# Performance work log

Hardware: AMD Instinct MI355X
Metric: run time of the kernel (lower is better)

The kernel has to match this reference:

```python
import jax, jax.numpy as jnp
import numpy as np

N, C, H, W = 8, 256, 128, 128   # images, AE-error channels, feature map size
A = 3                            # anchors per location (3 aspect ratios)
G = 64                           # GT boxes per image
STRIDE = 8
ANCHOR_SIZE = 32.0
ASPECT_RATIOS = (0.5, 1.0, 2.0)
UNK_CLASS = 80
D = 64                           # density_dim


def make_anchors():
    # detectron2 DefaultAnchorGenerator: cell anchors + grid shifts, (H, W, A) order, A fastest
    r = jnp.asarray(ASPECT_RATIOS, jnp.float32)
    w = ANCHOR_SIZE / jnp.sqrt(r)
    h = ANCHOR_SIZE * jnp.sqrt(r)
    cell = jnp.stack([-w / 2, -h / 2, w / 2, h / 2], axis=1)          # [A,4]
    sx = jnp.arange(W, dtype=jnp.float32) * STRIDE
    sy = jnp.arange(H, dtype=jnp.float32) * STRIDE
    yy, xx = jnp.meshgrid(sy, sx, indexing='ij')
    shifts = jnp.stack([xx, yy, xx, yy], axis=-1).reshape(-1, 4)      # [H*W,4]
    return (shifts[:, None, :] + cell[None, :, :]).reshape(-1, 4)     # [H*W*A,4]


def pairwise_iou(boxes, anchors):
    # boxes [G,4], anchors [R,4] -> [G,R]
    area_b = (boxes[:, 2] - boxes[:, 0]) * (boxes[:, 3] - boxes[:, 1])
    area_a = (anchors[:, 2] - anchors[:, 0]) * (anchors[:, 3] - anchors[:, 1])
    lt = jnp.maximum(boxes[:, None, :2], anchors[None, :, :2])
    rb = jnp.minimum(boxes[:, None, 2:], anchors[None, :, 2:])
    wh = jnp.clip(rb - lt, 0.0)
    inter = wh[..., 0] * wh[..., 1]
    return inter / jnp.maximum(area_b[:, None] + area_a[None, :] - inter, 1e-9)


def setup_inputs() -> dict:
    key = jax.random.key(0)
    k = jax.random.split(key, 9)
    err = jax.random.normal(k[0], (N, C, H, W), jnp.float32)
    err_map = jax.random.normal(k[1], (N, 1, H, W), jnp.float32)
    cxy = jax.random.uniform(k[2], (N, G, 2), minval=0.0, maxval=float(H * STRIDE))
    wh = jax.random.uniform(k[3], (N, G, 2), minval=16.0, maxval=128.0)
    gt_boxes = jnp.concatenate([cxy - wh / 2, cxy + wh / 2], axis=-1)
    gt_classes = jax.random.randint(k[4], (N, G), 0, 81, dtype=jnp.int32)
    w1 = jax.random.normal(k[5], (1, D), jnp.float32) * 0.5
    b1 = jnp.zeros((D,), jnp.float32)
    w2 = jax.random.normal(k[6], (D, D // 2), jnp.float32) * (1.0 / np.sqrt(D))
    b2 = jnp.zeros((D // 2,), jnp.float32)
    w3 = jax.random.normal(k[7], (D // 2, 1), jnp.float32) * (1.0 / np.sqrt(D // 2))
    b3 = jnp.zeros((1,), jnp.float32)
    return dict(err=err, err_map=err_map, gt_boxes=gt_boxes, w1=w1, b1=b1,
                w2=w2, b2=b2, w3=w3, b3=b3, gt_classes=gt_classes)


def reference(err, err_map, gt_boxes, w1, b1, w2, b2, w3, b3, gt_classes):
    # loss_ae: mean of squared flattened per-anchor errors (mean is permutation invariant)
    loss_ae = jnp.mean(err ** 2)

    # density head on every error-map pixel: Linear(1,D)-ReLU-Linear(D,D/2)-ReLU-Linear(D/2,1)
    pix = err_map.transpose(0, 2, 3, 1).reshape(N, H * W)              # [N,M]
    hmid = jax.nn.relu(pix[..., None] * w1[0] + b1)                    # [N,M,D]
    hmid = jax.nn.relu(jnp.einsum('nmd,de->nme', hmid, w2) + b2)       # [N,M,D/2]
    p_unk = (jnp.einsum('nme,eo->nmo', hmid, w3) + b3)[..., 0]         # [N,M]

    # anchor matching (torch.no_grad in original)
    anchors = make_anchors()                                           # [R,4]

    def match_one(boxes_i, classes_i):
        iou = pairwise_iou(boxes_i, anchors)                           # [G,R]
        idxs = jnp.argmax(iou, axis=0)                                 # per-anchor best GT
        return classes_i[idxs]                                         # [R]

    matched_classes = jax.vmap(match_one)(jax.lax.stop_gradient(gt_boxes), gt_classes)
    unk = (matched_classes == UNK_CLASS)                               # [N,R]
    mask = jnp.any(unk.reshape(N, H * W, A), axis=2).astype(jnp.float32)  # [N,M]

    # BCE with logits, mean reduction (stable form)
    loss_density = jnp.mean(jnp.logaddexp(0.0, p_unk) - p_unk * mask)
    return jnp.stack([loss_ae, loss_density])
```

## Files before the change

kernel.cpp:

```cpp
#include <hip/hip_runtime.h>
#include <math.h>

#define GNUM 64
#define DDIM 64
#define EDIM 32
#define UNK_CLASS 80
#define DBLK 512
#define ABLK 4096
#define NBLK (DBLK + ABLK)

__global__ __launch_bounds__(256) void fused_kernel(
    const float* __restrict__ err,
    const float* __restrict__ err_map,
    const float* __restrict__ gt_boxes,
    const float* __restrict__ w1,
    const float* __restrict__ b1,
    const float* __restrict__ w2,
    const float* __restrict__ b2,
    const float* __restrict__ w3,
    const float* __restrict__ b3,
    const int*   __restrict__ gt_classes,
    float* __restrict__ ws)
{
    const int t = threadIdx.x;
    const int b = blockIdx.x;
    float part = 0.0f;
    __shared__ float red[4];

    if (b >= DBLK) {
        const float4* __restrict__ e4 = (const float4*)err;
        const int base = (b - DBLK) * 2048 + t;
        float4 v0 = e4[base + 0*256];
        float4 v1 = e4[base + 1*256];
        float4 v2 = e4[base + 2*256];
        float4 v3 = e4[base + 3*256];
        float4 v4 = e4[base + 4*256];
        float4 v5 = e4[base + 5*256];
        float4 v6 = e4[base + 6*256];
        float4 v7 = e4[base + 7*256];
        float s0, s1, s2, s3;
        s0 = v0.x*v0.x; s1 = v0.y*v0.y; s2 = v0.z*v0.z; s3 = v0.w*v0.w;
        s0 = fmaf(v1.x,v1.x,s0); s1 = fmaf(v1.y,v1.y,s1); s2 = fmaf(v1.z,v1.z,s2); s3 = fmaf(v1.w,v1.w,s3);
        s0 = fmaf(v2.x,v2.x,s0); s1 = fmaf(v2.y,v2.y,s1); s2 = fmaf(v2.z,v2.z,s2); s3 = fmaf(v2.w,v2.w,s3);
        s0 = fmaf(v3.x,v3.x,s0); s1 = fmaf(v3.y,v3.y,s1); s2 = fmaf(v3.z,v3.z,s2); s3 = fmaf(v3.w,v3.w,s3);
        s0 = fmaf(v4.x,v4.x,s0); s1 = fmaf(v4.y,v4.y,s1); s2 = fmaf(v4.z,v4.z,s2); s3 = fmaf(v4.w,v4.w,s3);
        s0 = fmaf(v5.x,v5.x,s0); s1 = fmaf(v5.y,v5.y,s1); s2 = fmaf(v5.z,v5.z,s2); s3 = fmaf(v5.w,v5.w,s3);
        s0 = fmaf(v6.x,v6.x,s0); s1 = fmaf(v6.y,v6.y,s1); s2 = fmaf(v6.z,v6.z,s2); s3 = fmaf(v6.w,v6.w,s3);
        s0 = fmaf(v7.x,v7.x,s0); s1 = fmaf(v7.y,v7.y,s1); s2 = fmaf(v7.z,v7.z,s2); s3 = fmaf(v7.w,v7.w,s3);
        part = (s0+s1) + (s2+s3);
    } else {
        const int n  = b >> 6;
        const int m  = ((b & 63) << 8) | t;

        const float cx = (float)(m & 127) * 8.0f;
        const float cy = (float)(m >> 7) * 8.0f;
        const float s05 = sqrtf(0.5f), s2r = sqrtf(2.0f);
        const float hw0 = 0.5f*(32.0f/s05), hh0 = 0.5f*(32.0f*s05);
        const float hw1 = 16.0f,            hh1 = 16.0f;
        const float hw2 = 0.5f*(32.0f/s2r), hh2 = 0.5f*(32.0f*s2r);

        const float ax1[3] = {cx-hw0, cx-hw1, cx-hw2};
        const float ay1[3] = {cy-hh0, cy-hh1, cy-hh2};
        const float ax2[3] = {cx+hw0, cx+hw1, cx+hw2};
        const float ay2[3] = {cy+hh0, cy+hh1, cy+hh2};
        float areaA[3];
        #pragma unroll
        for (int a = 0; a < 3; ++a) areaA[a] = (ax2[a]-ax1[a])*(ay2[a]-ay1[a]);

        float bi[3] = {-1.f,-1.f,-1.f}, bd[3] = {1.f,1.f,1.f};
        int   idx[3] = {0,0,0};

        const float* __restrict__ bp = gt_boxes + n*GNUM*4;
        #pragma unroll 4
        for (int g = 0; g < GNUM; ++g) {
            const float bx1 = bp[4*g+0], by1 = bp[4*g+1];
            const float bx2 = bp[4*g+2], by2 = bp[4*g+3];
            const float areaB = (bx2-bx1)*(by2-by1);
            #pragma unroll
            for (int a = 0; a < 3; ++a) {
                float lx = fmaxf(bx1, ax1[a]), ly = fmaxf(by1, ay1[a]);
                float rx = fminf(bx2, ax2[a]), ry = fminf(by2, ay2[a]);
                float iw = fmaxf(rx-lx, 0.f),  ih = fmaxf(ry-ly, 0.f);
                float inter = iw*ih;
                float dn = fmaxf(areaB + areaA[a] - inter, 1e-9f);
                if (inter*bd[a] > bi[a]*dn) { bi[a]=inter; bd[a]=dn; idx[a]=g; }
            }
        }
        const int* __restrict__ cp = gt_classes + n*GNUM;
        const bool unk = (cp[idx[0]] == UNK_CLASS) |
                         (cp[idx[1]] == UNK_CLASS) |
                         (cp[idx[2]] == UNK_CLASS);
        const float mask = unk ? 1.0f : 0.0f;

        const float xv = err_map[(n << 14) + m];
        float acc[EDIM];
        #pragma unroll
        for (int e = 0; e < EDIM; ++e) acc[e] = b2[e];

        #pragma unroll 2
        for (int d = 0; d < DDIM; ++d) {
            const float h = fmaxf(fmaf(xv, w1[d], b1[d]), 0.0f);
            const float* __restrict__ wr = w2 + d*EDIM;
            #pragma unroll
            for (int e = 0; e < EDIM; ++e)
                acc[e] = fmaf(h, wr[e], acc[e]);
        }
        float p = b3[0];
        #pragma unroll
        for (int e = 0; e < EDIM; ++e)
            p = fmaf(fmaxf(acc[e], 0.0f), w3[e], p);

        part = fmaxf(p, 0.0f) + log1pf(expf(-fabsf(p))) - p*mask;
    }

    float x = part;
    #pragma unroll
    for (int off = 32; off > 0; off >>= 1) x += __shfl_xor(x, off, 64);
    if ((t & 63) == 0) red[t >> 6] = x;
    __syncthreads();
    if (t == 0) ws[b] = (red[0]+red[1]) + (red[2]+red[3]);
}

__global__ __launch_bounds__(256) void finalize_kernel(const float* __restrict__ ws,
                                                       float* __restrict__ out)
{
    const int t = threadIdx.x;
    float sd = 0.f, sa = 0.f;
    for (int i = t; i < DBLK; i += 256) sd += ws[i];
    for (int i = DBLK + t; i < NBLK; i += 256) sa += ws[i];
    #pragma unroll
    for (int off = 32; off > 0; off >>= 1) {
        sd += __shfl_xor(sd, off, 64);
        sa += __shfl_xor(sa, off, 64);
    }
    __shared__ float rd[4], ra[4];
    if ((t & 63) == 0) { rd[t >> 6] = sd; ra[t >> 6] = sa; }
    __syncthreads();
    if (t == 0) {
        out[0] = ((ra[0]+ra[1])+(ra[2]+ra[3])) * (1.0f/33554432.0f);
        out[1] = ((rd[0]+rd[1])+(rd[2]+rd[3])) * (1.0f/131072.0f);
    }
}

extern "C" void kernel_launch(void* const* d_in, const int* in_sizes, int n_in,
                              void* d_out, int out_size, void* d_ws, size_t ws_size,
                              hipStream_t stream) {
    const float* err        = (const float*)d_in[0];
    const float* err_map    = (const float*)d_in[1];
    const float* gt_boxes   = (const float*)d_in[2];
    const float* w1         = (const float*)d_in[3];
    const float* b1         = (const float*)d_in[4];
    const float* w2         = (const float*)d_in[5];
    const float* b2         = (const float*)d_in[6];
    const float* w3         = (const float*)d_in[7];
    const float* b3         = (const float*)d_in[8];
    const int*   gt_classes = (const int*)d_in[9];
    float* out = (float*)d_out;
    float* ws  = (float*)d_ws;

    fused_kernel<<<NBLK, 256, 0, stream>>>(err, err_map, gt_boxes, w1, b1, w2, b2,
                                           w3, b3, gt_classes, ws);
    finalize_kernel<<<1, 256, 0, stream>>>(ws, out);
}
```

Before: 222.0 us.

## Split density work across 4 lanes per pixel and interleave with AE blocks

Each pixel's density work (anchor-GT IoU matching plus the MLP) is now split across 4 lanes. Each lane handles 16 GT boxes and 8 hidden outputs, and the partial results are merged with cross-lane shuffles. Density blocks grow from 512 to 2048 and are interleaved 1:2 with the AE reduction blocks, so the compute-heavy and bandwidth-heavy blocks run concurrently instead of in two phases. The aim is to shorten the long per-thread serial chains and balance load across CUs. In exchange it adds shuffle overhead and recomputes the anchor setup four times per pixel.

```diff
diff --git a/kernel.cpp b/kernel.cpp
--- a/kernel.cpp
+++ b/kernel.cpp
@@ -5,7 +5,7 @@
 #define DDIM 64
 #define EDIM 32
 #define UNK_CLASS 80
-#define DBLK 512
+#define DBLK 2048
 #define ABLK 4096
 #define NBLK (DBLK + ABLK)
 
@@ -25,11 +25,14 @@
     const int t = threadIdx.x;
     const int b = blockIdx.x;
     float part = 0.0f;
+    int wsIdx;
     __shared__ float red[4];
 
-    if (b >= DBLK) {
+    if (b % 3 != 0) {
+        const int ab = b - b/3 - 1;
+        wsIdx = DBLK + ab;
         const float4* __restrict__ e4 = (const float4*)err;
-        const int base = (b - DBLK) * 2048 + t;
+        const int base = ab * 2048 + t;
         float4 v0 = e4[base + 0*256];
         float4 v1 = e4[base + 1*256];
         float4 v2 = e4[base + 2*256];
@@ -49,8 +52,13 @@
         s0 = fmaf(v7.x,v7.x,s0); s1 = fmaf(v7.y,v7.y,s1); s2 = fmaf(v7.z,v7.z,s2); s3 = fmaf(v7.w,v7.w,s3);
         part = (s0+s1) + (s2+s3);
     } else {
-        const int n  = b >> 6;
-        const int m  = ((b & 63) << 8) | t;
+        const int db   = b / 3;
+        wsIdx = db;
+        const int dtid = (db << 8) | t;
+        const int pix  = dtid >> 2;
+        const int q    = dtid & 3;
+        const int n    = pix >> 14;
+        const int m    = pix & 16383;
 
         const float cx = (float)(m & 127) * 8.0f;
         const float cy = (float)(m >> 7) * 8.0f;
@@ -70,47 +78,65 @@
         float bi[3] = {-1.f,-1.f,-1.f}, bd[3] = {1.f,1.f,1.f};
         int   idx[3] = {0,0,0};
 
-        const float* __restrict__ bp = gt_boxes + n*GNUM*4;
+        const float4* __restrict__ bp = (const float4*)(gt_boxes + n*GNUM*4);
         #pragma unroll 4
-        for (int g = 0; g < GNUM; ++g) {
-            const float bx1 = bp[4*g+0], by1 = bp[4*g+1];
-            const float bx2 = bp[4*g+2], by2 = bp[4*g+3];
-            const float areaB = (bx2-bx1)*(by2-by1);
+        for (int i = 0; i < 16; ++i) {
+            const int g = (q << 4) | i;
+            const float4 bx = bp[g];
+            const float areaB = (bx.z-bx.x)*(bx.w-bx.y);
             #pragma unroll
             for (int a = 0; a < 3; ++a) {
-                float lx = fmaxf(bx1, ax1[a]), ly = fmaxf(by1, ay1[a]);
-                float rx = fminf(bx2, ax2[a]), ry = fminf(by2, ay2[a]);
-                float iw = fmaxf(rx-lx, 0.f),  ih = fmaxf(ry-ly, 0.f);
+                float lx = fmaxf(bx.x, ax1[a]), ly = fmaxf(bx.y, ay1[a]);
+                float rx = fminf(bx.z, ax2[a]), ry = fminf(bx.w, ay2[a]);
+                float iw = fmaxf(rx-lx, 0.f),   ih = fmaxf(ry-ly, 0.f);
                 float inter = iw*ih;
                 float dn = fmaxf(areaB + areaA[a] - inter, 1e-9f);
                 if (inter*bd[a] > bi[a]*dn) { bi[a]=inter; bd[a]=dn; idx[a]=g; }
+            }
+        }
+        #pragma unroll
+        for (int mask = 1; mask <= 2; mask <<= 1) {
+            #pragma unroll
+            for (int a = 0; a < 3; ++a) {
+                float ri = __shfl_xor(bi[a], mask, 64);
+                float rd = __shfl_xor(bd[a], mask, 64);
+                int   rx = __shfl_xor(idx[a], mask, 64);
+                float lhs = ri*bd[a], rhs = bi[a]*rd;
+                bool take = (lhs > rhs) || ((lhs == rhs) && (rx < idx[a]));
+                if (take) { bi[a]=ri; bd[a]=rd; idx[a]=rx; }
             }
         }
         const int* __restrict__ cp = gt_classes + n*GNUM;
         const bool unk = (cp[idx[0]] == UNK_CLASS) |
                          (cp[idx[1]] == UNK_CLASS) |
                          (cp[idx[2]] == UNK_CLASS);
-        const float mask = unk ? 1.0f : 0.0f;
+        const float mask01 = unk ? 1.0f : 0.0f;
 
-        const float xv = err_map[(n << 14) + m];
-        float acc[EDIM];
-        #pragma unroll
-        for (int e = 0; e < EDIM; ++e) acc[e] = b2[e];
-
-        #pragma unroll 2
+        const float xv = err_map[pix];
+        float acc[8] = {0,0,0,0,0,0,0,0};
+        const float4* __restrict__ w2v = (const float4*)(w2 + (q << 3));
+        #pragma unroll 4
         for (int d = 0; d < DDIM; ++d) {
             const float h = fmaxf(fmaf(xv, w1[d], b1[d]), 0.0f);
-            const float* __restrict__ wr = w2 + d*EDIM;
-            #pragma unroll
-            for (int e = 0; e < EDIM; ++e)
-                acc[e] = fmaf(h, wr[e], acc[e]);
+            const float4 wa = w2v[d*8 + 0];
+            const float4 wb = w2v[d*8 + 1];
+            acc[0] = fmaf(h, wa.x, acc[0]); acc[1] = fmaf(h, wa.y, acc[1]);
+            acc[2] = fmaf(h, wa.z, acc[2]); acc[3] = fmaf(h, wa.w, acc[3]);
+            acc[4] = fmaf(h, wb.x, acc[4]); acc[5] = fmaf(h, wb.y, acc[5]);
+            acc[6] = fmaf(h, wb.z, acc[6]); acc[7] = fmaf(h, wb.w, acc[7]);
         }
-        float p = b3[0];
+        float pq = 0.0f;
         #pragma unroll
-        for (int e = 0; e < EDIM; ++e)
-            p = fmaf(fmaxf(acc[e], 0.0f), w3[e], p);
+        for (int j = 0; j < 8; ++j) {
+            const int e = (q << 3) + j;
+            pq = fmaf(fmaxf(acc[j] + b2[e], 0.0f), w3[e], pq);
+        }
+        pq += __shfl_xor(pq, 1, 64);
+        pq += __shfl_xor(pq, 2, 64);
+        const float p = pq + b3[0];
 
-        part = fmaxf(p, 0.0f) + log1pf(expf(-fabsf(p))) - p*mask;
+        if (q == 0)
+            part = fmaxf(p, 0.0f) + log1pf(expf(-fabsf(p))) - p*mask01;
     }
 
     float x = part;
@@ -118,7 +144,7 @@
     for (int off = 32; off > 0; off >>= 1) x += __shfl_xor(x, off, 64);
     if ((t & 63) == 0) red[t >> 6] = x;
     __syncthreads();
-    if (t == 0) ws[b] = (red[0]+red[1]) + (red[2]+red[3]);
+    if (t == 0) ws[wsIdx] = (red[0]+red[1]) + (red[2]+red[3]);
 }
 
 __global__ __launch_bounds__(256) void finalize_kernel(const float* __restrict__ ws,
```

New measurement: 245.1 us. 1.1x slower.
